# Performance work log

Hardware: AMD Instinct MI355X
Metric: run time of the kernel (lower is better)

The kernel has to match this reference:

```python
import jax, jax.numpy as jnp
import numpy as np

N_NODES = 2048
N_GRAPHS = 64
N_EDGES = 16384
B = 65536
META = 64
TX = 8
NOISE = 128
IN_DIM = N_NODES + 1 + 32 + TX  # 2089


def setup_inputs() -> dict:
    key = jax.random.key(0)
    ks = jax.random.split(key, 11)
    return {
        "batched_graphs": jax.random.randint(ks[0], (B,), 0, N_GRAPHS),
        "batched_chain": jax.random.normal(ks[1], (B,), dtype=jnp.float32),
        "trigger_data": jax.random.normal(ks[2], (B, META), dtype=jnp.float32),
        "tx_start_time": jax.random.normal(ks[3], (B, TX), dtype=jnp.float32),
        "edges": jax.random.randint(ks[4], (N_GRAPHS, 2, N_EDGES), 0, N_NODES),
        "gcn_w": jax.random.normal(ks[5], (), dtype=jnp.float32),
        "gcn_b": jax.random.normal(ks[6], (), dtype=jnp.float32) * 0.01,
        "trig_W": jax.random.normal(ks[7], (META, 32), dtype=jnp.float32) / np.sqrt(META),
        "trig_b": jnp.zeros((32,), dtype=jnp.float32),
        "emb_W": jax.random.normal(ks[8], (IN_DIM, NOISE), dtype=jnp.float32) / np.sqrt(IN_DIM),
        "emb_b": jnp.zeros((NOISE,), dtype=jnp.float32),
    }


def _gcn_one_graph(edge_index, w, b):
    # GCNConv(1,1) on x = ones(n_nodes,1): add self loops, sym-normalize.
    self_idx = jnp.arange(N_NODES, dtype=edge_index.dtype)
    src = jnp.concatenate([edge_index[0], self_idx])
    dst = jnp.concatenate([edge_index[1], self_idx])
    deg = jax.ops.segment_sum(jnp.ones(src.shape[0], jnp.float32), dst,
                              num_segments=N_NODES)
    dinv = jnp.where(deg > 0, jax.lax.rsqrt(deg), 0.0)
    norm = dinv[src] * dinv[dst]
    agg = jax.ops.segment_sum(norm, dst, num_segments=N_NODES)  # [n_nodes]
    return agg * w + b  # x @ W with x==1 is just w per node, plus bias


def reference(batched_graphs, batched_chain, trigger_data, tx_start_time,
              edges, gcn_w, gcn_b, trig_W, trig_b, emb_W, emb_b):
    # Per-graph GCN embeddings for all topologies (covers all uniques). [G, n_nodes]
    graph_emb = jax.vmap(lambda e: _gcn_one_graph(e, gcn_w, gcn_b))(edges)
    ge = graph_emb[batched_graphs]                         # [B, n_nodes] gather
    trig = jax.nn.relu(trigger_data @ trig_W + trig_b)     # [B, 32]
    x = jnp.concatenate(
        [ge, batched_chain[:, None], trig, tx_start_time], axis=1)  # [B, IN_DIM]
    return x @ emb_W + emb_b                               # [B, NOISE]
```

## Files before the change

### kernel.cpp

```cpp
#include <hip/hip_runtime.h>

#define NN 2048
#define NG 64
#define NE 16384
#define BB 65536
#define META 64
#define TXD 8
#define NOISE 128


__global__ __launch_bounds__(256) void agg_kernel(
    const int* __restrict__ edges,
    const float* __restrict__ gcn_w,
    const float* __restrict__ gcn_b,
    float* __restrict__ emb,
    float* __restrict__ graph_out)
{
    __shared__ int                s_cnt[NN];
    __shared__ float              s_dinv[NN];
    __shared__ unsigned long long s_acc[NN];
    const int g = blockIdx.x, tid = threadIdx.x;
    const int4* __restrict__ e4 = (const int4*)(edges + (size_t)g * 2 * NE);

    if (tid < NOISE) graph_out[g * NOISE + tid] = 0.0f;

    int4 ds[16];
    #pragma unroll
    for (int k = 0; k < 16; ++k) ds[k] = e4[4096 + k * 256 + tid];

    for (int n = tid; n < NN; n += 256) { s_cnt[n] = 1; s_acc[n] = 0ull; }
    __syncthreads();

    #pragma unroll
    for (int k = 0; k < 16; ++k) {
        atomicAdd(&s_cnt[ds[k].x], 1);
        atomicAdd(&s_cnt[ds[k].y], 1);
        atomicAdd(&s_cnt[ds[k].z], 1);
        atomicAdd(&s_cnt[ds[k].w], 1);
    }
    __syncthreads();
    for (int n = tid; n < NN; n += 256) s_dinv[n] = rsqrtf((float)s_cnt[n]);
    __syncthreads();

    const float SCALE = 1099511627776.0f;
    #pragma unroll
    for (int k = 0; k < 16; ++k) {
        int4 sr = e4[k * 256 + tid];
        float nx = s_dinv[sr.x] * s_dinv[ds[k].x];
        float ny = s_dinv[sr.y] * s_dinv[ds[k].y];
        float nz = s_dinv[sr.z] * s_dinv[ds[k].z];
        float nw = s_dinv[sr.w] * s_dinv[ds[k].w];
        atomicAdd(&s_acc[ds[k].x], (unsigned long long)(nx * SCALE));
        atomicAdd(&s_acc[ds[k].y], (unsigned long long)(ny * SCALE));
        atomicAdd(&s_acc[ds[k].z], (unsigned long long)(nz * SCALE));
        atomicAdd(&s_acc[ds[k].w], (unsigned long long)(nw * SCALE));
    }
    __syncthreads();

    const float w = gcn_w[0], b = gcn_b[0];
    for (int n = tid; n < NN; n += 256) {
        float di = s_dinv[n];
        float agg = (float)((double)s_acc[n] * 0x1p-40) + di * di;
        emb[(size_t)g * NN + n] = agg * w + b;
    }
}

__global__ __launch_bounds__(256) void fold_kernel(
    const float* __restrict__ emb,
    const float* __restrict__ emb_W,
    float* __restrict__ graph_out)
{
    __shared__ float s_e[128];
    __shared__ float s_red[128];
    const int tid = threadIdx.x;
    const int g = blockIdx.x >> 4, chunk = blockIdx.x & 15;
    const int n0 = chunk * 128;
    if (tid < 128) s_e[tid] = emb[(size_t)g * NN + n0 + tid];
    __syncthreads();
    const int c = tid & 127, h = tid >> 7;
    const float* __restrict__ Wp = emb_W + (size_t)(n0 + h * 64) * NOISE + c;
    const float* __restrict__ ep = s_e + h * 64;
    float a0 = 0.f, a1 = 0.f, a2 = 0.f, a3 = 0.f;
    #pragma unroll
    for (int i = 0; i < 64; i += 4) {
        a0 = fmaf(ep[i + 0], Wp[(i + 0) * NOISE], a0);
        a1 = fmaf(ep[i + 1], Wp[(i + 1) * NOISE], a1);
        a2 = fmaf(ep[i + 2], Wp[(i + 2) * NOISE], a2);
        a3 = fmaf(ep[i + 3], Wp[(i + 3) * NOISE], a3);
    }
    float acc = (a0 + a1) + (a2 + a3);
    if (h == 1) s_red[c] = acc;
    __syncthreads();
    if (h == 0) atomicAdd(&graph_out[g * NOISE + c], acc + s_red[c]);
}

#define ROWS 32
__global__ __launch_bounds__(256, 3) void main_kernel(
    const int* __restrict__ bg,
    const float* __restrict__ chain,
    const float* __restrict__ trig_in,
    const float* __restrict__ txs,
    const float* __restrict__ trig_W,
    const float* __restrict__ trig_b,
    const float* __restrict__ emb_W,
    const float* __restrict__ emb_b,
    const float* __restrict__ graph_out,
    float* __restrict__ out)
{
    __shared__ float s_td[ROWS * 68];
    __shared__ float s_twT[32 * 68];
    __shared__ float s_trig[ROWS * 36];
    __shared__ float s_tx[ROWS * TXD];
    __shared__ float s_ch[ROWS];
    __shared__ int   s_gi[ROWS];

    const int tid = threadIdx.x;
    const int row0 = blockIdx.x * ROWS;

    {
        const float4* __restrict__ gsrc =
            (const float4*)(trig_in + (size_t)row0 * META);
        #pragma unroll
        for (int k = 0; k < 2; ++k) {
            int t = tid + k * 256;
            int r = t >> 4, i4 = t & 15;
            *(float4*)&s_td[r * 68 + i4 * 4] = gsrc[t];
        }
    }
    {
        const float4* __restrict__ gsrc = (const float4*)trig_W;
        #pragma unroll
        for (int k = 0; k < 2; ++k) {
            int t = tid + k * 256;
            int i = t >> 3, j4 = (t & 7) * 4;
            float4 v = gsrc[t];
            s_twT[(j4 + 0) * 68 + i] = v.x;
            s_twT[(j4 + 1) * 68 + i] = v.y;
            s_twT[(j4 + 2) * 68 + i] = v.z;
            s_twT[(j4 + 3) * 68 + i] = v.w;
        }
    }
    if (tid < 64) {
        int r = tid >> 1, k4 = (tid & 1) * 4;
        *(float4*)&s_tx[r * TXD + k4] =
            ((const float4*)(txs + (size_t)row0 * TXD))[tid];
    } else if (tid < 96) {
        int r = tid - 64;
        s_ch[r] = chain[row0 + r];
    } else if (tid < 128) {
        int r = tid - 96;
        s_gi[r] = bg[row0 + r];
    }

    const int n0 = (tid & 63) * 2;
    float2 w2[32], w3[TXD];
    #pragma unroll
    for (int j = 0; j < 32; ++j)
        w2[j] = *(const float2*)&emb_W[(size_t)(2049 + j) * NOISE + n0];
    #pragma unroll
    for (int k = 0; k < TXD; ++k)
        w3[k] = *(const float2*)&emb_W[(size_t)(2081 + k) * NOISE + n0];
    const float2 w1   = *(const float2*)&emb_W[(size_t)2048 * NOISE + n0];
    const float2 bias = *(const float2*)&emb_b[n0];

    __syncthreads();

    {
        const int j0 = tid & 15;
        const int r0 = (tid >> 4) * 2;
        const float* __restrict__ tw0 = s_twT + j0 * 68;
        const float* __restrict__ tw1 = s_twT + (j0 + 16) * 68;
        const float* __restrict__ td0 = s_td + r0 * 68;
        const float* __restrict__ td1 = s_td + (r0 + 1) * 68;
        float b0 = trig_b[j0], b1 = trig_b[j0 + 16];
        float a00 = b0, a01 = b1, a10 = b0, a11 = b1;
        #pragma unroll
        for (int i = 0; i < META; i += 4) {
            float4 u0 = *(const float4*)(tw0 + i);
            float4 u1 = *(const float4*)(tw1 + i);
            float4 t0 = *(const float4*)(td0 + i);
            float4 t1 = *(const float4*)(td1 + i);
            a00 = fmaf(t0.x, u0.x, a00); a00 = fmaf(t0.y, u0.y, a00);
            a00 = fmaf(t0.z, u0.z, a00); a00 = fmaf(t0.w, u0.w, a00);
            a01 = fmaf(t0.x, u1.x, a01); a01 = fmaf(t0.y, u1.y, a01);
            a01 = fmaf(t0.z, u1.z, a01); a01 = fmaf(t0.w, u1.w, a01);
            a10 = fmaf(t1.x, u0.x, a10); a10 = fmaf(t1.y, u0.y, a10);
            a10 = fmaf(t1.z, u0.z, a10); a10 = fmaf(t1.w, u0.w, a10);
            a11 = fmaf(t1.x, u1.x, a11); a11 = fmaf(t1.y, u1.y, a11);
            a11 = fmaf(t1.z, u1.z, a11); a11 = fmaf(t1.w, u1.w, a11);
        }
        s_trig[r0 * 36 + j0]            = fmaxf(a00, 0.f);
        s_trig[r0 * 36 + j0 + 16]       = fmaxf(a01, 0.f);
        s_trig[(r0 + 1) * 36 + j0]      = fmaxf(a10, 0.f);
        s_trig[(r0 + 1) * 36 + j0 + 16] = fmaxf(a11, 0.f);
    }
    __syncthreads();

    const int wv = tid >> 6;
    int   gs[8];
    float chs[8];
    #pragma unroll
    for (int p = 0; p < 8; ++p) {
        const int r = p * 4 + wv;
        gs[p]  = s_gi[r];
        chs[p] = s_ch[r];
    }
    float2 go[8];
    #pragma unroll
    for (int p = 0; p < 8; ++p)
        go[p] = *(const float2*)&graph_out[gs[p] * NOISE + n0];

    #pragma unroll
    for (int p = 0; p < 8; ++p) {
        const int r = p * 4 + wv;
        const int row = row0 + r;
        float ax = bias.x + go[p].x + chs[p] * w1.x;
        float ay = bias.y + go[p].y + chs[p] * w1.y;
        const float4* __restrict__ tx4 = (const float4*)(s_tx + r * TXD);
        float4 t0 = tx4[0], t1 = tx4[1];
        ax = fmaf(t0.x, w3[0].x, ax); ay = fmaf(t0.x, w3[0].y, ay);
        ax = fmaf(t0.y, w3[1].x, ax); ay = fmaf(t0.y, w3[1].y, ay);
        ax = fmaf(t0.z, w3[2].x, ax); ay = fmaf(t0.z, w3[2].y, ay);
        ax = fmaf(t0.w, w3[3].x, ax); ay = fmaf(t0.w, w3[3].y, ay);
        ax = fmaf(t1.x, w3[4].x, ax); ay = fmaf(t1.x, w3[4].y, ay);
        ax = fmaf(t1.y, w3[5].x, ax); ay = fmaf(t1.y, w3[5].y, ay);
        ax = fmaf(t1.z, w3[6].x, ax); ay = fmaf(t1.z, w3[6].y, ay);
        ax = fmaf(t1.w, w3[7].x, ax); ay = fmaf(t1.w, w3[7].y, ay);
        const float* __restrict__ tg = s_trig + r * 36;
        #pragma unroll
        for (int q = 0; q < 8; ++q) {
            float4 t4 = *(const float4*)(tg + q * 4);
            ax = fmaf(t4.x, w2[4 * q + 0].x, ax); ay = fmaf(t4.x, w2[4 * q + 0].y, ay);
            ax = fmaf(t4.y, w2[4 * q + 1].x, ax); ay = fmaf(t4.y, w2[4 * q + 1].y, ay);
            ax = fmaf(t4.z, w2[4 * q + 2].x, ax); ay = fmaf(t4.z, w2[4 * q + 2].y, ay);
            ax = fmaf(t4.w, w2[4 * q + 3].x, ax); ay = fmaf(t4.w, w2[4 * q + 3].y, ay);
        }
        *(float2*)&out[(size_t)row * NOISE + n0] = make_float2(ax, ay);
    }
}

extern "C" void kernel_launch(void* const* d_in, const int* in_sizes, int n_in,
                              void* d_out, int out_size, void* d_ws, size_t ws_size,
                              hipStream_t stream) {
    const int*   bg      = (const int*)d_in[0];
    const float* chain   = (const float*)d_in[1];
    const float* trig_in = (const float*)d_in[2];
    const float* txs     = (const float*)d_in[3];
    const int*   edges   = (const int*)d_in[4];
    const float* gcn_w   = (const float*)d_in[5];
    const float* gcn_b   = (const float*)d_in[6];
    const float* trig_W  = (const float*)d_in[7];
    const float* trig_b  = (const float*)d_in[8];
    const float* emb_W   = (const float*)d_in[9];
    const float* emb_b   = (const float*)d_in[10];
    float* out = (float*)d_out;

    float* graph_out = (float*)d_ws;
    float* emb       = (float*)d_ws + NG * NOISE;

    agg_kernel<<<NG, 256, 0, stream>>>(edges, gcn_w, gcn_b, emb, graph_out);
    fold_kernel<<<NG * 16, 256, 0, stream>>>(emb, emb_W, graph_out);
    main_kernel<<<BB / ROWS, 256, 0, stream>>>(bg, chain, trig_in, txs, trig_W,
                                               trig_b, emb_W, emb_b, graph_out, out);
}
```

Measured before the change: 130.3 us.

## Fuse GCN aggregation with emb_W fold and widen main kernel to float4 columns

```diff
diff --git a/kernel.cpp b/kernel.cpp
--- a/kernel.cpp
+++ b/kernel.cpp
@@ -9,20 +9,19 @@
 #define NOISE 128
 
 
-__global__ __launch_bounds__(256) void agg_kernel(
+__global__ __launch_bounds__(256) void agg_fold_kernel(
     const int* __restrict__ edges,
     const float* __restrict__ gcn_w,
     const float* __restrict__ gcn_b,
-    float* __restrict__ emb,
+    const float* __restrict__ emb_W,
     float* __restrict__ graph_out)
 {
     __shared__ int                s_cnt[NN];
-    __shared__ float              s_dinv[NN];
+    __shared__ float              s_emb[NN];
     __shared__ unsigned long long s_acc[NN];
+    __shared__ float              s_part[8][NOISE];
     const int g = blockIdx.x, tid = threadIdx.x;
     const int4* __restrict__ e4 = (const int4*)(edges + (size_t)g * 2 * NE);
-
-    if (tid < NOISE) graph_out[g * NOISE + tid] = 0.0f;
 
     int4 ds[16];
     #pragma unroll
@@ -39,17 +38,17 @@
         atomicAdd(&s_cnt[ds[k].w], 1);
     }
     __syncthreads();
-    for (int n = tid; n < NN; n += 256) s_dinv[n] = rsqrtf((float)s_cnt[n]);
+    for (int n = tid; n < NN; n += 256) s_emb[n] = rsqrtf((float)s_cnt[n]);
     __syncthreads();
 
     const float SCALE = 1099511627776.0f;
     #pragma unroll
     for (int k = 0; k < 16; ++k) {
         int4 sr = e4[k * 256 + tid];
-        float nx = s_dinv[sr.x] * s_dinv[ds[k].x];
-        float ny = s_dinv[sr.y] * s_dinv[ds[k].y];
-        float nz = s_dinv[sr.z] * s_dinv[ds[k].z];
-        float nw = s_dinv[sr.w] * s_dinv[ds[k].w];
+        float nx = s_emb[sr.x] * s_emb[ds[k].x];
+        float ny = s_emb[sr.y] * s_emb[ds[k].y];
+        float nz = s_emb[sr.z] * s_emb[ds[k].z];
+        float nw = s_emb[sr.w] * s_emb[ds[k].w];
         atomicAdd(&s_acc[ds[k].x], (unsigned long long)(nx * SCALE));
         atomicAdd(&s_acc[ds[k].y], (unsigned long long)(ny * SCALE));
         atomicAdd(&s_acc[ds[k].z], (unsigned long long)(nz * SCALE));
@@ -59,43 +58,46 @@
 
     const float w = gcn_w[0], b = gcn_b[0];
     for (int n = tid; n < NN; n += 256) {
-        float di = s_dinv[n];
+        float di = s_emb[n];
         float agg = (float)((double)s_acc[n] * 0x1p-40) + di * di;
-        emb[(size_t)g * NN + n] = agg * w + b;
+        s_emb[n] = agg * w + b;
+    }
+    __syncthreads();
+
+    {
+        const int cg = tid & 31, seg = tid >> 5;
+        const int c4 = cg * 4;
+        const int nbase = seg * 256;
+        float4 acc = make_float4(0.f, 0.f, 0.f, 0.f);
+        #pragma unroll 4
+        for (int i = 0; i < 256; i += 4) {
+            float4 e = *(const float4*)&s_emb[nbase + i];
+            float4 w0 = *(const float4*)&emb_W[(size_t)(nbase + i + 0) * NOISE + c4];
+            float4 w1 = *(const float4*)&emb_W[(size_t)(nbase + i + 1) * NOISE + c4];
+            float4 w2 = *(const float4*)&emb_W[(size_t)(nbase + i + 2) * NOISE + c4];
+            float4 w3 = *(const float4*)&emb_W[(size_t)(nbase + i + 3) * NOISE + c4];
+            acc.x = fmaf(e.x, w0.x, acc.x); acc.y = fmaf(e.x, w0.y, acc.y);
+            acc.z = fmaf(e.x, w0.z, acc.z); acc.w = fmaf(e.x, w0.w, acc.w);
+            acc.x = fmaf(e.y, w1.x, acc.x); acc.y = fmaf(e.y, w1.y, acc.y);
+            acc.z = fmaf(e.y, w1.z, acc.z); acc.w = fmaf(e.y, w1.w, acc.w);
+            acc.x = fmaf(e.z, w2.x, acc.x); acc.y = fmaf(e.z, w2.y, acc.y);
+            acc.z = fmaf(e.z, w2.z, acc.z); acc.w = fmaf(e.z, w2.w, acc.w);
+            acc.x = fmaf(e.w, w3.x, acc.x); acc.y = fmaf(e.w, w3.y, acc.y);
+            acc.z = fmaf(e.w, w3.z, acc.z); acc.w = fmaf(e.w, w3.w, acc.w);
+        }
+        *(float4*)&s_part[seg][c4] = acc;
+    }
+    __syncthreads();
+    if (tid < NOISE) {
+        float s = 0.f;
+        #pragma unroll
+        for (int k = 0; k < 8; ++k) s += s_part[k][tid];
+        graph_out[g * NOISE + tid] = s;
     }
 }
 
-__global__ __launch_bounds__(256) void fold_kernel(
-    const float* __restrict__ emb,
-    const float* __restrict__ emb_W,
-    float* __restrict__ graph_out)
-{
-    __shared__ float s_e[128];
-    __shared__ float s_red[128];
-    const int tid = threadIdx.x;
-    const int g = blockIdx.x >> 4, chunk = blockIdx.x & 15;
-    const int n0 = chunk * 128;
-    if (tid < 128) s_e[tid] = emb[(size_t)g * NN + n0 + tid];
-    __syncthreads();
-    const int c = tid & 127, h = tid >> 7;
-    const float* __restrict__ Wp = emb_W + (size_t)(n0 + h * 64) * NOISE + c;
-    const float* __restrict__ ep = s_e + h * 64;
-    float a0 = 0.f, a1 = 0.f, a2 = 0.f, a3 = 0.f;
-    #pragma unroll
-    for (int i = 0; i < 64; i += 4) {
-        a0 = fmaf(ep[i + 0], Wp[(i + 0) * NOISE], a0);
-        a1 = fmaf(ep[i + 1], Wp[(i + 1) * NOISE], a1);
-        a2 = fmaf(ep[i + 2], Wp[(i + 2) * NOISE], a2);
-        a3 = fmaf(ep[i + 3], Wp[(i + 3) * NOISE], a3);
-    }
-    float acc = (a0 + a1) + (a2 + a3);
-    if (h == 1) s_red[c] = acc;
-    __syncthreads();
-    if (h == 0) atomicAdd(&graph_out[g * NOISE + c], acc + s_red[c]);
-}
-
 #define ROWS 32
-__global__ __launch_bounds__(256, 3) void main_kernel(
+__global__ __launch_bounds__(256, 2) void main_kernel(
     const int* __restrict__ bg,
     const float* __restrict__ chain,
     const float* __restrict__ trig_in,
@@ -152,16 +154,16 @@
         s_gi[r] = bg[row0 + r];
     }
 
-    const int n0 = (tid & 63) * 2;
-    float2 w2[32], w3[TXD];
+    const int n0 = (tid & 31) * 4;
+    float4 w2[32], w3[TXD];
     #pragma unroll
     for (int j = 0; j < 32; ++j)
-        w2[j] = *(const float2*)&emb_W[(size_t)(2049 + j) * NOISE + n0];
+        w2[j] = *(const float4*)&emb_W[(size_t)(2049 + j) * NOISE + n0];
     #pragma unroll
     for (int k = 0; k < TXD; ++k)
-        w3[k] = *(const float2*)&emb_W[(size_t)(2081 + k) * NOISE + n0];
-    const float2 w1   = *(const float2*)&emb_W[(size_t)2048 * NOISE + n0];
-    const float2 bias = *(const float2*)&emb_b[n0];
+        w3[k] = *(const float4*)&emb_W[(size_t)(2081 + k) * NOISE + n0];
+    const float4 w1   = *(const float4*)&emb_W[(size_t)2048 * NOISE + n0];
+    const float4 bias = *(const float4*)&emb_b[n0];
 
     __syncthreads();
 
@@ -196,46 +198,60 @@
     }
     __syncthreads();
 
-    const int wv = tid >> 6;
-    int   gs[8];
-    float chs[8];
-    #pragma unroll
-    for (int p = 0; p < 8; ++p) {
-        const int r = p * 4 + wv;
+    const int rg = tid >> 5;
+    int   gs[4];
+    float chs[4];
+    #pragma unroll
+    for (int p = 0; p < 4; ++p) {
+        const int r = p * 8 + rg;
         gs[p]  = s_gi[r];
         chs[p] = s_ch[r];
     }
-    float2 go[8];
-    #pragma unroll
-    for (int p = 0; p < 8; ++p)
-        go[p] = *(const float2*)&graph_out[gs[p] * NOISE + n0];
-
-    #pragma unroll
-    for (int p = 0; p < 8; ++p) {
-        const int r = p * 4 + wv;
+    float4 go[4];
+    #pragma unroll
+    for (int p = 0; p < 4; ++p)
+        go[p] = *(const float4*)&graph_out[gs[p] * NOISE + n0];
+
+    #pragma unroll
+    for (int p = 0; p < 4; ++p) {
+        const int r = p * 8 + rg;
         const int row = row0 + r;
         float ax = bias.x + go[p].x + chs[p] * w1.x;
         float ay = bias.y + go[p].y + chs[p] * w1.y;
+        float az = bias.z + go[p].z + chs[p] * w1.z;
+        float aw = bias.w + go[p].w + chs[p] * w1.w;
         const float4* __restrict__ tx4 = (const float4*)(s_tx + r * TXD);
         float4 t0 = tx4[0], t1 = tx4[1];
         ax = fmaf(t0.x, w3[0].x, ax); ay = fmaf(t0.x, w3[0].y, ay);
+        az = fmaf(t0.x, w3[0].z, az); aw = fmaf(t0.x, w3[0].w, aw);
         ax = fmaf(t0.y, w3[1].x, ax); ay = fmaf(t0.y, w3[1].y, ay);
+        az = fmaf(t0.y, w3[1].z, az); aw = fmaf(t0.y, w3[1].w, aw);
         ax = fmaf(t0.z, w3[2].x, ax); ay = fmaf(t0.z, w3[2].y, ay);
+        az = fmaf(t0.z, w3[2].z, az); aw = fmaf(t0.z, w3[2].w, aw);
         ax = fmaf(t0.w, w3[3].x, ax); ay = fmaf(t0.w, w3[3].y, ay);
+        az = fmaf(t0.w, w3[3].z, az); aw = fmaf(t0.w, w3[3].w, aw);
         ax = fmaf(t1.x, w3[4].x, ax); ay = fmaf(t1.x, w3[4].y, ay);
+        az = fmaf(t1.x, w3[4].z, az); aw = fmaf(t1.x, w3[4].w, aw);
         ax = fmaf(t1.y, w3[5].x, ax); ay = fmaf(t1.y, w3[5].y, ay);
+        az = fmaf(t1.y, w3[5].z, az); aw = fmaf(t1.y, w3[5].w, aw);
         ax = fmaf(t1.z, w3[6].x, ax); ay = fmaf(t1.z, w3[6].y, ay);
+        az = fmaf(t1.z, w3[6].z, az); aw = fmaf(t1.z, w3[6].w, aw);
         ax = fmaf(t1.w, w3[7].x, ax); ay = fmaf(t1.w, w3[7].y, ay);
+        az = fmaf(t1.w, w3[7].z, az); aw = fmaf(t1.w, w3[7].w, aw);
         const float* __restrict__ tg = s_trig + r * 36;
         #pragma unroll
         for (int q = 0; q < 8; ++q) {
             float4 t4 = *(const float4*)(tg + q * 4);
             ax = fmaf(t4.x, w2[4 * q + 0].x, ax); ay = fmaf(t4.x, w2[4 * q + 0].y, ay);
+            az = fmaf(t4.x, w2[4 * q + 0].z, az); aw = fmaf(t4.x, w2[4 * q + 0].w, aw);
             ax = fmaf(t4.y, w2[4 * q + 1].x, ax); ay = fmaf(t4.y, w2[4 * q + 1].y, ay);
+            az = fmaf(t4.y, w2[4 * q + 1].z, az); aw = fmaf(t4.y, w2[4 * q + 1].w, aw);
             ax = fmaf(t4.z, w2[4 * q + 2].x, ax); ay = fmaf(t4.z, w2[4 * q + 2].y, ay);
+            az = fmaf(t4.z, w2[4 * q + 2].z, az); aw = fmaf(t4.z, w2[4 * q + 2].w, aw);
             ax = fmaf(t4.w, w2[4 * q + 3].x, ax); ay = fmaf(t4.w, w2[4 * q + 3].y, ay);
-        }
-        *(float2*)&out[(size_t)row * NOISE + n0] = make_float2(ax, ay);
+            az = fmaf(t4.w, w2[4 * q + 3].z, az); aw = fmaf(t4.w, w2[4 * q + 3].w, aw);
+        }
+        *(float4*)&out[(size_t)row * NOISE + n0] = make_float4(ax, ay, az, aw);
     }
 }
 
@@ -256,10 +272,8 @@
     float* out = (float*)d_out;
 
     float* graph_out = (float*)d_ws;
-    float* emb       = (float*)d_ws + NG * NOISE;
-
-    agg_kernel<<<NG, 256, 0, stream>>>(edges, gcn_w, gcn_b, emb, graph_out);
-    fold_kernel<<<NG * 16, 256, 0, stream>>>(emb, emb_W, graph_out);
+
+    agg_fold_kernel<<<NG, 256, 0, stream>>>(edges, gcn_w, gcn_b, emb_W, graph_out);
     main_kernel<<<BB / ROWS, 256, 0, stream>>>(bg, chain, trig_in, txs, trig_W,
                                                trig_b, emb_W, emb_b, graph_out, out);
 }
```

After: 138.6 us. 6.4% more time.
